# Performance work log

Hardware: AMD Instinct MI355X
Metric: run time of the kernel (lower is better)

The kernel has to match this reference:

```python
import jax, jax.numpy as jnp
import numpy as np

N = 20000
E = 640000
C_IN = 256
C_OUT = 256
K = 2
EPS = 1e-12


def setup_inputs() -> dict:
    key = jax.random.key(0)
    k1, k2, k3, k4, k5 = jax.random.split(key, 5)
    x = jax.random.normal(k1, (N, C_IN), dtype=jnp.float32)
    edge_index = jax.random.randint(k2, (2, E), 0, N, dtype=jnp.int64)
    edge_weights = jax.random.uniform(k3, (E,), dtype=jnp.float32)
    lin_w = jax.random.normal(k4, (C_OUT, C_IN), dtype=jnp.float32) / np.sqrt(C_IN)
    lin_b = jax.random.normal(k5, (C_OUT,), dtype=jnp.float32) * 0.01
    return {"x": x, "edge_index": edge_index, "edge_weights": edge_weights,
            "lin_w": lin_w, "lin_b": lin_b}


def reference(x, edge_index, edge_weights, lin_w, lin_b):
    row, col = edge_index[0], edge_index[1]  # source -> target

    # F.normalize(x, p=2, dim=-1)
    nrm = jnp.sqrt(jnp.sum(x * x, axis=-1, keepdims=True))
    x = x / jnp.maximum(nrm, EPS)

    # gcn_norm with add_self_loops=False (PyG): deg over target nodes
    deg = jax.ops.segment_sum(edge_weights, col, num_segments=N)
    deg_inv_sqrt = jnp.where(deg > 0, 1.0 / jnp.sqrt(deg), 0.0)
    norm = deg_inv_sqrt[row] * edge_weights * deg_inv_sqrt[col]  # [E]

    # K-hop propagation: out[col] += norm * x[row]
    for _ in range(K):
        msgs = norm[:, None] * x[row]                     # [E, C]
        x = jax.ops.segment_sum(msgs, col, num_segments=N)

    # Linear layer of SGConv
    return x @ lin_w.T + lin_b
```

## Files before the change

### kernel.cpp

```cpp
#include <hip/hip_runtime.h>
#include <hip/hip_bf16.h>

#define N_NODES 20000
#define N_EDGES 640000
#define C 256
#define S 96
#define CNTS 16

#define SCATTER_BLOCKS 2500
#define WCONV_BLOCKS 256
#define NORM_BLOCKS 10000

#define BPAD 264

typedef __attribute__((ext_vector_type(8))) short short8;
typedef __attribute__((ext_vector_type(4))) float float4v;
typedef __attribute__((ext_vector_type(4))) unsigned uint4v;

__device__ inline unsigned short f2bf(float f) {
    unsigned u = __float_as_uint(f);
    unsigned r = (u + 0x7fffu + ((u >> 16) & 1u)) >> 16;
    return (unsigned short)r;
}
__device__ inline float bf_lo(unsigned u) { return __uint_as_float(u << 16); }
__device__ inline float bf_hi(unsigned u) { return __uint_as_float(u & 0xffff0000u); }
__device__ inline float bf_hi_raw(unsigned u) { return __uint_as_float(u); }

__global__ __launch_bounds__(256) void scatter_kernel(
        const int* __restrict__ ei, const float* __restrict__ w,
        const float* __restrict__ lw,
        int* __restrict__ cnt, unsigned* __restrict__ csr,
        unsigned short* __restrict__ Wb) {
    int b = blockIdx.x;
    int t = threadIdx.x;
    if (b < SCATTER_BLOCKS) {
        __shared__ int okw[4];
        unsigned long long m = __ballot(ei[2 * t + 1] == 0);
        if ((t & 63) == 0) okw[t >> 6] = (m == 0xFFFFFFFFFFFFFFFFull) ? 1 : 0;
        __syncthreads();
        int flag = okw[0] & okw[1] & okw[2] & okw[3];
        int e = b * 256 + t;
        int r, c;
        if (flag) { r = ei[2 * e]; c = ei[2 * (N_EDGES + e)]; }
        else      { r = ei[e];     c = ei[N_EDGES + e]; }
        int pos = atomicAdd(&cnt[c * CNTS], 1);
        if (pos < S) csr[c * S + pos] = (unsigned)r | ((unsigned)f2bf(w[e]) << 16);
    } else {
        int idx = (b - SCATTER_BLOCKS) * 256 + t;
        Wb[idx] = f2bf(lw[idx]);
    }
}

__global__ __launch_bounds__(256) void norm_kernel(
        const float* __restrict__ x, const unsigned* __restrict__ csr,
        const int* __restrict__ cnt,
        float* __restrict__ dis, unsigned char* __restrict__ ncap,
        unsigned* __restrict__ xs32) {
    int t = threadIdx.x;
    int half = t >> 7;
    int tt = t & 127;
    int i = blockIdx.x * 2 + half;
    int n = cnt[i * CNTS];
    if (n > S) n = S;
    float2 v = ((const float2*)x)[(size_t)i * 128 + tt];
    float ss = v.x * v.x + v.y * v.y;
    float sd = (tt < n) ? bf_hi(csr[i * S + tt]) : 0.0f;
    #pragma unroll
    for (int o = 32; o > 0; o >>= 1) {
        ss += __shfl_down(ss, o, 64);
        sd += __shfl_down(sd, o, 64);
    }
    __shared__ float2 wsum[4];
    if ((t & 63) == 0) wsum[t >> 6] = make_float2(ss, sd);
    __syncthreads();
    float tot = wsum[half * 2].x + wsum[half * 2 + 1].x;
    float deg = wsum[half * 2].y + wsum[half * 2 + 1].y;
    float d = (deg > 0.0f) ? rsqrtf(deg) : 0.0f;
    float inv = d / fmaxf(sqrtf(tot), 1e-12f);
    xs32[(size_t)i * 128 + tt] =
        (unsigned)f2bf(v.x * inv) | ((unsigned)f2bf(v.y * inv) << 16);
    if (tt == 0) {
        dis[i] = d;
        ncap[i] = (unsigned char)n;
    }
}

#define MAC4(ee, vv)                                              \
    {   float wf = __uint_as_float(ee.y);                         \
        c0.x += wf * bf_lo(vv.x); c0.y += wf * bf_hi_raw(vv.x);   \
        c1.x += wf * bf_lo(vv.y); c1.y += wf * bf_hi_raw(vv.y);   \
        c2.x += wf * bf_lo(vv.z); c2.y += wf * bf_hi_raw(vv.z);   \
        c3.x += wf * bf_lo(vv.w); c3.y += wf * bf_hi_raw(vv.w); }

template <int POW>
__global__ __launch_bounds__(256) void gather_kernel(const unsigned char* __restrict__ ncap,
                                                     const unsigned* __restrict__ csr,
                                                     const float* __restrict__ dis,
                                                     const unsigned* __restrict__ in,
                                                     unsigned* __restrict__ out) {
    __shared__ uint2 st_all[4][S];
    int wvi = threadIdx.x >> 6;
    int lane = threadIdx.x & 63;
    int i = blockIdx.x * 4 + wvi;
    int n = ncap[i];
    int nup = (n + 7) & ~7;
    uint2* st = st_all[wvi];
    if (lane < n) {
        unsigned p = __builtin_nontemporal_load(&csr[i * S + lane]);
        st[lane] = make_uint2((p & 0xffffu) << 9, p & 0xffff0000u);
    }
    if (lane + 64 < n) {
        unsigned p = __builtin_nontemporal_load(&csr[i * S + lane + 64]);
        st[lane + 64] = make_uint2((p & 0xffffu) << 9, p & 0xffff0000u);
    }
    {
        int k = n + lane;
        if (k < nup) st[k] = make_uint2(0u, 0u);
    }
    __builtin_amdgcn_wave_barrier();

    int grp = lane >> 5;
    unsigned hb = (unsigned)(lane & 31) << 4;
    const char* base = (const char*)in;
    float2 c0 = {0.f, 0.f}, c1 = {0.f, 0.f}, c2 = {0.f, 0.f}, c3 = {0.f, 0.f};
    int j = 0;
    for (; j + 16 <= nup; j += 16) {
        uint2 e0 = st[j + grp];
        uint2 e1 = st[j + 2 + grp];
        uint2 e2 = st[j + 4 + grp];
        uint2 e3 = st[j + 6 + grp];
        uint2 e4 = st[j + 8 + grp];
        uint2 e5 = st[j + 10 + grp];
        uint2 e6 = st[j + 12 + grp];
        uint2 e7 = st[j + 14 + grp];
        uint4v v0 = *(const uint4v*)(base + (e0.x + hb));
        uint4v v1 = *(const uint4v*)(base + (e1.x + hb));
        uint4v v2 = *(const uint4v*)(base + (e2.x + hb));
        uint4v v3 = *(const uint4v*)(base + (e3.x + hb));
        uint4v v4 = *(const uint4v*)(base + (e4.x + hb));
        uint4v v5 = *(const uint4v*)(base + (e5.x + hb));
        uint4v v6 = *(const uint4v*)(base + (e6.x + hb));
        uint4v v7 = *(const uint4v*)(base + (e7.x + hb));
        MAC4(e0, v0) MAC4(e1, v1) MAC4(e2, v2) MAC4(e3, v3)
        MAC4(e4, v4) MAC4(e5, v5) MAC4(e6, v6) MAC4(e7, v7)
    }
    if (j < nup) {
        uint2 e0 = st[j + grp];
        uint2 e1 = st[j + 2 + grp];
        uint2 e2 = st[j + 4 + grp];
        uint2 e3 = st[j + 6 + grp];
        uint4v v0 = *(const uint4v*)(base + (e0.x + hb));
        uint4v v1 = *(const uint4v*)(base + (e1.x + hb));
        uint4v v2 = *(const uint4v*)(base + (e2.x + hb));
        uint4v v3 = *(const uint4v*)(base + (e3.x + hb));
        MAC4(e0, v0) MAC4(e1, v1) MAC4(e2, v2) MAC4(e3, v3)
    }
    c0.x += __shfl_down(c0.x, 32, 64); c0.y += __shfl_down(c0.y, 32, 64);
    c1.x += __shfl_down(c1.x, 32, 64); c1.y += __shfl_down(c1.y, 32, 64);
    c2.x += __shfl_down(c2.x, 32, 64); c2.y += __shfl_down(c2.y, 32, 64);
    c3.x += __shfl_down(c3.x, 32, 64); c3.y += __shfl_down(c3.y, 32, 64);
    if (lane < 32) {
        float d = dis[i];
        float sc = (POW == 2) ? d * d : d;
        uint4v r;
        r.x = (unsigned)f2bf(c0.x * sc) | ((unsigned)f2bf(c0.y * sc) << 16);
        r.y = (unsigned)f2bf(c1.x * sc) | ((unsigned)f2bf(c1.y * sc) << 16);
        r.z = (unsigned)f2bf(c2.x * sc) | ((unsigned)f2bf(c2.y * sc) << 16);
        r.w = (unsigned)f2bf(c3.x * sc) | ((unsigned)f2bf(c3.y * sc) << 16);
        __builtin_nontemporal_store(r, (uint4v*)(out + (size_t)i * 128) + lane);
    }
}

__global__ __launch_bounds__(256, 4) void gemm_kernel(const unsigned short* __restrict__ h,
                                                      const unsigned short* __restrict__ Wb,
                                                      const float* __restrict__ b,
                                                      float* __restrict__ out) {
    __shared__ unsigned short Bs[64 * BPAD];
    int t = threadIdx.x;
    int wv = t >> 6;
    int lane = t & 63;
    int m = lane & 15;
    int q = lane >> 4;
    int rg = blockIdx.x >> 2;
    int cg = blockIdx.x & 3;
    #pragma unroll
    for (int it = 0; it < 8; it++) {
        int ch = it * 256 + t;
        int col = ch >> 5;
        int off8 = (ch & 31) * 8;
        *(uint4v*)(Bs + col * BPAD + off8) =
            *(const uint4v*)(Wb + (size_t)(cg * 64 + col) * C + off8);
    }
    __syncthreads();

    int rowbase = rg * 64 + wv * 16;
    int rowA = rowbase + m;
    if (rowA > N_NODES - 1) rowA = N_NODES - 1;
    float4v acc[4];
    #pragma unroll
    for (int nt = 0; nt < 4; nt++) acc[nt] = (float4v){0.f, 0.f, 0.f, 0.f};
    #pragma unroll
    for (int kt = 0; kt < 8; kt++) {
        int kb = kt * 32 + q * 8;
        short8 a = *(const short8*)(h + (size_t)rowA * C + kb);
        #pragma unroll
        for (int nt = 0; nt < 4; nt++) {
            short8 bb = *(const short8*)(Bs + (nt * 16 + m) * BPAD + kb);
            acc[nt] = __builtin_amdgcn_mfma_f32_16x16x32_bf16(a, bb, acc[nt], 0, 0, 0);
        }
    }
    #pragma unroll
    for (int nt = 0; nt < 4; nt++) {
        int col = cg * 64 + nt * 16 + m;
        float bias = b[col];
        #pragma unroll
        for (int r = 0; r < 4; r++) {
            int ro = rowbase + q * 4 + r;
            if (ro < N_NODES)
                __builtin_nontemporal_store(acc[nt][r] + bias, &out[(size_t)ro * C + col]);
        }
    }
}

extern "C" void kernel_launch(void* const* d_in, const int* in_sizes, int n_in,
                              void* d_out, int out_size, void* d_ws, size_t ws_size,
                              hipStream_t stream) {
    const float* x  = (const float*)d_in[0];
    const int*   ei = (const int*)d_in[1];
    const float* w  = (const float*)d_in[2];
    const float* lw = (const float*)d_in[3];
    const float* lb = (const float*)d_in[4];
    float* out = (float*)d_out;

    char* ws = (char*)d_ws;
    size_t off = 0;
    auto alloc = [&](size_t bytes) -> void* {
        void* p = ws + off;
        off = (off + bytes + 255) & ~(size_t)255;
        return p;
    };
    unsigned* bufA   = (unsigned*)alloc((size_t)N_NODES * 128 * 4);
    unsigned* bufB   = (unsigned*)alloc((size_t)N_NODES * 128 * 4);
    float* dis       = (float*)alloc((size_t)N_NODES * 4);
    int*   cnt       = (int*)alloc((size_t)N_NODES * CNTS * 4);
    unsigned* csr    = (unsigned*)alloc((size_t)N_NODES * S * 4);
    unsigned short* Wb = (unsigned short*)alloc((size_t)C * C * 2);
    unsigned char* ncap = (unsigned char*)alloc((size_t)N_NODES);
    (void)ws_size; (void)in_sizes; (void)n_in; (void)out_size;

    (void)hipMemsetAsync(cnt, 0, (size_t)N_NODES * CNTS * 4, stream);

    scatter_kernel<<<SCATTER_BLOCKS + WCONV_BLOCKS, 256, 0, stream>>>(
        ei, w, lw, cnt, csr, Wb);
    norm_kernel<<<NORM_BLOCKS, 256, 0, stream>>>(x, csr, cnt, dis, ncap, bufA);
    gather_kernel<2><<<N_NODES / 4, 256, 0, stream>>>(ncap, csr, dis, bufA, bufB);
    gather_kernel<1><<<N_NODES / 4, 256, 0, stream>>>(ncap, csr, dis, bufB, bufA);
    gemm_kernel<<<313 * 4, 256, 0, stream>>>(
        (const unsigned short*)bufA, Wb, lb, out);
}
```

Baseline: 197.1 us.

## Split gather feature dimension across two waves per node with 4-way edge groups

The gather kernel now assigns two wavefronts per destination node, each handling half of the 256 bf16 channels. Within a wave, lanes form four edge groups of 16 lanes instead of two groups of 32, and the partial sums are reduced with an extra shuffle stage. The grid doubles and neighbor feature loads become nontemporal. This raises parallelism and memory-level parallelism per node, but each wave now loads the CSR list redundantly, does more reduction work, and issues fewer loads per unrolled iteration.

New measurement: 228.6 us. 16.0% more time.

```diff
diff --git a/kernel.cpp b/kernel.cpp
--- a/kernel.cpp
+++ b/kernel.cpp
@@ -101,9 +101,11 @@
     __shared__ uint2 st_all[4][S];
     int wvi = threadIdx.x >> 6;
     int lane = threadIdx.x & 63;
-    int i = blockIdx.x * 4 + wvi;
+    int i = blockIdx.x * 2 + (wvi >> 1);
+    int chalf = wvi & 1;
+    float d = dis[i];
     int n = ncap[i];
-    int nup = (n + 7) & ~7;
+    int nup = (n + 3) & ~3;
     uint2* st = st_all[wvi];
     if (lane < n) {
         unsigned p = __builtin_nontemporal_load(&csr[i * S + lane]);
@@ -119,55 +121,44 @@
     }
     __builtin_amdgcn_wave_barrier();
 
-    int grp = lane >> 5;
-    unsigned hb = (unsigned)(lane & 31) << 4;
+    int grp = lane >> 4;
+    unsigned hb = ((unsigned)(lane & 15) << 4) + ((unsigned)chalf << 8);
     const char* base = (const char*)in;
     float2 c0 = {0.f, 0.f}, c1 = {0.f, 0.f}, c2 = {0.f, 0.f}, c3 = {0.f, 0.f};
     int j = 0;
     for (; j + 16 <= nup; j += 16) {
         uint2 e0 = st[j + grp];
-        uint2 e1 = st[j + 2 + grp];
-        uint2 e2 = st[j + 4 + grp];
-        uint2 e3 = st[j + 6 + grp];
-        uint2 e4 = st[j + 8 + grp];
-        uint2 e5 = st[j + 10 + grp];
-        uint2 e6 = st[j + 12 + grp];
-        uint2 e7 = st[j + 14 + grp];
-        uint4v v0 = *(const uint4v*)(base + (e0.x + hb));
-        uint4v v1 = *(const uint4v*)(base + (e1.x + hb));
-        uint4v v2 = *(const uint4v*)(base + (e2.x + hb));
-        uint4v v3 = *(const uint4v*)(base + (e3.x + hb));
-        uint4v v4 = *(const uint4v*)(base + (e4.x + hb));
-        uint4v v5 = *(const uint4v*)(base + (e5.x + hb));
-        uint4v v6 = *(const uint4v*)(base + (e6.x + hb));
-        uint4v v7 = *(const uint4v*)(base + (e7.x + hb));
+        uint2 e1 = st[j + 4 + grp];
+        uint2 e2 = st[j + 8 + grp];
+        uint2 e3 = st[j + 12 + grp];
+        uint4v v0 = __builtin_nontemporal_load((const uint4v*)(base + (e0.x + hb)));
+        uint4v v1 = __builtin_nontemporal_load((const uint4v*)(base + (e1.x + hb)));
+        uint4v v2 = __builtin_nontemporal_load((const uint4v*)(base + (e2.x + hb)));
+        uint4v v3 = __builtin_nontemporal_load((const uint4v*)(base + (e3.x + hb)));
         MAC4(e0, v0) MAC4(e1, v1) MAC4(e2, v2) MAC4(e3, v3)
-        MAC4(e4, v4) MAC4(e5, v5) MAC4(e6, v6) MAC4(e7, v7)
-    }
-    if (j < nup) {
+    }
+    for (; j < nup; j += 4) {
         uint2 e0 = st[j + grp];
-        uint2 e1 = st[j + 2 + grp];
-        uint2 e2 = st[j + 4 + grp];
-        uint2 e3 = st[j + 6 + grp];
-        uint4v v0 = *(const uint4v*)(base + (e0.x + hb));
-        uint4v v1 = *(const uint4v*)(base + (e1.x + hb));
-        uint4v v2 = *(const uint4v*)(base + (e2.x + hb));
-        uint4v v3 = *(const uint4v*)(base + (e3.x + hb));
-        MAC4(e0, v0) MAC4(e1, v1) MAC4(e2, v2) MAC4(e3, v3)
+        uint4v v0 = __builtin_nontemporal_load((const uint4v*)(base + (e0.x + hb)));
+        MAC4(e0, v0)
     }
     c0.x += __shfl_down(c0.x, 32, 64); c0.y += __shfl_down(c0.y, 32, 64);
     c1.x += __shfl_down(c1.x, 32, 64); c1.y += __shfl_down(c1.y, 32, 64);
     c2.x += __shfl_down(c2.x, 32, 64); c2.y += __shfl_down(c2.y, 32, 64);
     c3.x += __shfl_down(c3.x, 32, 64); c3.y += __shfl_down(c3.y, 32, 64);
-    if (lane < 32) {
-        float d = dis[i];
+    c0.x += __shfl_down(c0.x, 16, 64); c0.y += __shfl_down(c0.y, 16, 64);
+    c1.x += __shfl_down(c1.x, 16, 64); c1.y += __shfl_down(c1.y, 16, 64);
+    c2.x += __shfl_down(c2.x, 16, 64); c2.y += __shfl_down(c2.y, 16, 64);
+    c3.x += __shfl_down(c3.x, 16, 64); c3.y += __shfl_down(c3.y, 16, 64);
+    if (lane < 16) {
         float sc = (POW == 2) ? d * d : d;
         uint4v r;
         r.x = (unsigned)f2bf(c0.x * sc) | ((unsigned)f2bf(c0.y * sc) << 16);
         r.y = (unsigned)f2bf(c1.x * sc) | ((unsigned)f2bf(c1.y * sc) << 16);
         r.z = (unsigned)f2bf(c2.x * sc) | ((unsigned)f2bf(c2.y * sc) << 16);
         r.w = (unsigned)f2bf(c3.x * sc) | ((unsigned)f2bf(c3.y * sc) << 16);
-        __builtin_nontemporal_store(r, (uint4v*)(out + (size_t)i * 128) + lane);
+        __builtin_nontemporal_store(
+            r, (uint4v*)(out + (size_t)i * 128 + chalf * 64) + lane);
     }
 }
 
@@ -253,8 +244,8 @@
     scatter_kernel<<<SCATTER_BLOCKS + WCONV_BLOCKS, 256, 0, stream>>>(
         ei, w, lw, cnt, csr, Wb);
     norm_kernel<<<NORM_BLOCKS, 256, 0, stream>>>(x, csr, cnt, dis, ncap, bufA);
-    gather_kernel<2><<<N_NODES / 4, 256, 0, stream>>>(ncap, csr, dis, bufA, bufB);
-    gather_kernel<1><<<N_NODES / 4, 256, 0, stream>>>(ncap, csr, dis, bufB, bufA);
+    gather_kernel<2><<<N_NODES / 2, 256, 0, stream>>>(ncap, csr, dis, bufA, bufB);
+    gather_kernel<1><<<N_NODES / 2, 256, 0, stream>>>(ncap, csr, dis, bufB, bufA);
     gemm_kernel<<<313 * 4, 256, 0, stream>>>(
         (const unsigned short*)bufA, Wb, lb, out);
 }
```
